# Performance work log

Measured on AMD Instinct MI355X. Metric: run time of the kernel, lower is better.

## Reference

```python
import jax, jax.numpy as jnp
import numpy as np

H = 8          # query heads
KVH = 1        # key/value heads
HD = 256       # head dim
ROPE_BASE = 10000.0


def _rotate_half(x):
    x1, x2 = x[..., : HD // 2], x[..., HD // 2 :]
    return jnp.concatenate((-x2, x1), axis=-1)


def _rope_cos_sin(position_ids):
    # position_ids: [B, S] int -> cos/sin: [B, S, HD]
    inv_freq = 1.0 / (ROPE_BASE ** (jnp.arange(0, HD, 2, dtype=jnp.float32) / HD))
    freqs = position_ids.astype(jnp.float32)[..., None] * inv_freq  # [B,S,HD/2]
    emb = jnp.concatenate((freqs, freqs), axis=-1)                  # [B,S,HD]
    return jnp.cos(emb), jnp.sin(emb)


def setup_inputs() -> dict:
    key = jax.random.key(0)
    ks = jax.random.split(key, 5)
    B, S, D = 2, 2048, 2048
    return {
        "hidden_states": jax.random.normal(ks[0], (B, S, D), dtype=jnp.float32),
        "attention_mask": jnp.zeros((B, 1, S, S), dtype=jnp.float32),
        "position_ids": jnp.broadcast_to(jnp.arange(S, dtype=jnp.int32), (B, S)),
        "Wq": jax.random.normal(ks[1], (D, H * HD), dtype=jnp.float32) * 0.02,
        "Wk": jax.random.normal(ks[2], (D, KVH * HD), dtype=jnp.float32) * 0.02,
        "Wv": jax.random.normal(ks[3], (D, KVH * HD), dtype=jnp.float32) * 0.02,
        "Wo": jax.random.normal(ks[4], (H * HD, D), dtype=jnp.float32) * 0.02,
    }


def reference(hidden_states, attention_mask, position_ids, Wq, Wk, Wv, Wo):
    B, S, D = hidden_states.shape
    # projections -> [B, heads, S, HD]
    q = jnp.einsum("bsd,df->bsf", hidden_states, Wq).reshape(B, S, H, HD).transpose(0, 2, 1, 3)
    k = jnp.einsum("bsd,df->bsf", hidden_states, Wk).reshape(B, S, KVH, HD).transpose(0, 2, 1, 3)
    v = jnp.einsum("bsd,df->bsf", hidden_states, Wv).reshape(B, S, KVH, HD).transpose(0, 2, 1, 3)

    cos, sin = _rope_cos_sin(position_ids)
    cos, sin = cos[:, None], sin[:, None]  # unsqueeze head dim
    q = q * cos + _rotate_half(q) * sin
    k = k * cos + _rotate_half(k) * sin

    # GQA: repeat kv heads to match query heads
    rep = H // KVH
    k = jnp.repeat(k, rep, axis=1)
    v = jnp.repeat(v, rep, axis=1)

    d_k = D // H  # matches torch code's scaling (== HD here)
    scores = jnp.einsum("bhqd,bhkd->bhqk", q, k) / jnp.sqrt(jnp.float32(d_k))
    scores = scores + attention_mask
    attn = jax.nn.softmax(scores, axis=-1)  # dropout p=0 / eval mode

    out = jnp.einsum("bhqk,bhkd->bhqd", attn, v)  # [B,H,S,HD]
    out = out.transpose(0, 2, 1, 3).reshape(B, S, H * HD)
    out = jnp.einsum("bsf,fd->bsd", out, Wo)
    return out
```

## Files before the change

### kernel.cpp

```cpp
#include <hip/hip_runtime.h>
#include <cmath>


typedef __bf16 bf16;
typedef __attribute__((ext_vector_type(8))) __bf16 bf16x8;
typedef __attribute__((ext_vector_type(4))) __bf16 bf16x4;
typedef __attribute__((ext_vector_type(4))) float f32x4;

#define S_LEN 2048
#define D_MODEL 2048
#define H_NUM 8
#define HDIM 256
#define NT (S_LEN / 64)
#define SM_BIAS 8.0f

#define BAR __builtin_amdgcn_s_barrier()
#define SCHED0 __builtin_amdgcn_sched_barrier(0)

__device__ __forceinline__ void gl_lds16(const bf16* g, bf16* l) {
  __builtin_amdgcn_global_load_lds(
      (const __attribute__((address_space(1))) void*)g,
      (__attribute__((address_space(3))) void*)l, 16, 0, 0);
}

__global__ void cvt_bf16(const float* __restrict__ src, bf16* __restrict__ dst) {
  const int i = (blockIdx.x * 256 + threadIdx.x) * 4;
  const float4 v = *(const float4*)(src + i);
  bf16x4 o;
  o[0] = (bf16)v.x; o[1] = (bf16)v.y; o[2] = (bf16)v.z; o[3] = (bf16)v.w;
  *(bf16x4*)(dst + i) = o;
}

__global__ void tpose_all(const float* __restrict__ Wq, const float* __restrict__ Wk,
                          const float* __restrict__ Wv, const float* __restrict__ Wo,
                          bf16* __restrict__ Wqkvt, bf16* __restrict__ Wot) {
  __shared__ float t[32][33];
  const int tx = threadIdx.x, ty = threadIdx.y;
  const int bx = blockIdx.x;
  const int k0 = blockIdx.y * 32;
  const float* W; bf16* Wt; int Ncols, no0, n0;
  if (bx < 64)      { W = Wq; Wt = Wqkvt; Ncols = 2048; no0 = 0;    n0 = bx * 32; }
  else if (bx < 72) { W = Wk; Wt = Wqkvt; Ncols = 256;  no0 = 2048; n0 = (bx - 64) * 32; }
  else if (bx < 80) { W = Wv; Wt = Wqkvt; Ncols = 256;  no0 = 2304; n0 = (bx - 72) * 32; }
  else              { W = Wo; Wt = Wot;   Ncols = 2048; no0 = 0;    n0 = (bx - 80) * 32; }
#pragma unroll
  for (int i = 0; i < 4; ++i)
    t[ty + 8 * i][tx] = W[(size_t)(k0 + ty + 8 * i) * Ncols + (n0 + tx)];
  __syncthreads();
#pragma unroll
  for (int i = 0; i < 4; ++i)
    Wt[(size_t)(no0 + n0 + ty + 8 * i) * D_MODEL + (k0 + tx)] = (bf16)t[tx][ty + 8 * i];
}

__global__ __launch_bounds__(512, 2)
void gemm_bf16(const bf16* __restrict__ A, const bf16* __restrict__ Wt,
               bf16* __restrict__ Cq, bf16* __restrict__ Ck, bf16* __restrict__ Cv,
               float* __restrict__ Cf, int NX, int mode) {
  __shared__ bf16 As[2][2][128 * 64];
  __shared__ bf16 Bs[2][2][128 * 64];
  const int tid = threadIdx.x;
  const int lane = tid & 63;
  const int w = tid >> 6;
  const int c16 = lane & 15;
  const int quad = lane >> 4;
  const int wm = w >> 2;
  const int wn = w & 3;

  const int nwg = gridDim.x;
  const int swz = (blockIdx.x & 7) * (nwg >> 3) + (blockIdx.x >> 3);
  const int m0 = (swz / NX) * 256;
  const int n0 = (swz % NX) * 256;

  const char* Ab = (const char*)A;
  const char* Bb = (const char*)Wt;
  const int lr8 = lane >> 3;
  const int scb = ((lane & 7) ^ lr8) << 4;

  f32x4 acc[8][4];
#pragma unroll
  for (int i = 0; i < 8; ++i)
#pragma unroll
    for (int j = 0; j < 4; ++j)
#pragma unroll
      for (int r = 0; r < 4; ++r) acc[i][j][r] = 0.f;

  auto stg = [&](const char* gcol, int grow0, bf16* lhalf) {
#pragma unroll
    for (int j2 = 0; j2 < 2; ++j2) {
      const int c = w * 2 + j2;
      gl_lds16((const bf16*)(gcol + (size_t)(grow0 + c * 8 + lr8) * 4096 + scb),
               lhalf + c * 512);
    }
  };
  auto ldA = [&](int sl, int qm, bf16x8* d) {
    const char* base = (const char*)&As[sl][wm][0];
#pragma unroll
    for (int i = 0; i < 4; ++i) {
      const int row = qm * 64 + i * 16 + c16;
      const int sw = (row & 7) << 4;
#pragma unroll
      for (int kk = 0; kk < 2; ++kk)
        d[i * 2 + kk] = *(const bf16x8*)(base + row * 128 + ((kk * 64 + quad * 16) ^ sw));
    }
  };
  auto ldB = [&](int sl, int qn, bf16x8* d) {
    const char* base = (const char*)&Bs[sl][wn >> 1][0];
#pragma unroll
    for (int j = 0; j < 2; ++j) {
      const int row = (wn & 1) * 64 + qn * 32 + j * 16 + c16;
      const int sw = (row & 7) << 4;
#pragma unroll
      for (int kk = 0; kk < 2; ++kk)
        d[j * 2 + kk] = *(const bf16x8*)(base + row * 128 + ((kk * 64 + quad * 16) ^ sw));
    }
  };
  auto mm = [&](int qm, int qn, const bf16x8* a, const bf16x8* bb) {
    __builtin_amdgcn_s_setprio(1);
#pragma unroll
    for (int kk = 0; kk < 2; ++kk)
#pragma unroll
      for (int i = 0; i < 4; ++i)
#pragma unroll
        for (int j = 0; j < 2; ++j)
          acc[qm * 4 + i][qn * 2 + j] = __builtin_amdgcn_mfma_f32_16x16x32_bf16(
              a[i * 2 + kk], bb[j * 2 + kk], acc[qm * 4 + i][qn * 2 + j], 0, 0, 0);
    __builtin_amdgcn_s_setprio(0);
  };

  bf16x8 Xa[8], Ya[8], Xb[4], Yb[4];

  stg(Ab, m0, &As[0][0][0]);        stg(Ab, m0 + 128, &As[0][1][0]);
  stg(Bb, n0, &Bs[0][0][0]);        stg(Bb, n0 + 128, &Bs[0][1][0]);
  stg(Bb + 128, n0, &Bs[1][0][0]);  stg(Bb + 128, n0 + 128, &Bs[1][1][0]);
  asm volatile("s_waitcnt vmcnt(4)" ::: "memory");
  BAR;

  for (int t = 0; t < 16; ++t) {
    const int kc = t * 256;
    const bool pf = (t < 15);
    ldA(0, 0, Xa); ldB(0, 0, Xb);
    stg(Ab + kc + 128, m0, &As[1][0][0]);
    BAR; mm(0, 0, Xa, Xb);
    ldB(0, 1, Yb);
    stg(Ab + kc + 128, m0 + 128, &As[1][1][0]);
    BAR; mm(0, 1, Xa, Yb);
    ldA(0, 1, Ya);
    if (pf) stg(Bb + kc + 256, n0, &Bs[0][0][0]);
    BAR; mm(1, 1, Ya, Yb);
    if (pf) {
      stg(Ab + kc + 256, m0, &As[0][0][0]);
      asm volatile("s_waitcnt vmcnt(4)" ::: "memory");
    } else {
      asm volatile("s_waitcnt vmcnt(0)" ::: "memory");
    }
    BAR; mm(1, 0, Ya, Xb);
    ldA(1, 0, Xa); ldB(1, 0, Xb);
    if (pf) stg(Bb + kc + 256, n0 + 128, &Bs[0][1][0]);
    BAR; mm(0, 0, Xa, Xb);
    ldB(1, 1, Yb);
    if (pf) stg(Ab + kc + 256, m0 + 128, &As[0][1][0]);
    BAR; mm(0, 1, Xa, Yb);
    ldA(1, 1, Ya);
    if (pf) stg(Bb + kc + 384, n0, &Bs[1][0][0]);
    BAR; mm(1, 1, Ya, Yb);
    if (pf) {
      stg(Bb + kc + 384, n0 + 128, &Bs[1][1][0]);
      asm volatile("s_waitcnt vmcnt(4)" ::: "memory");
      BAR; mm(1, 0, Ya, Xb);
    } else {
      BAR; mm(1, 0, Ya, Xb);
    }
  }

#pragma unroll
  for (int i = 0; i < 8; ++i)
#pragma unroll
    for (int j = 0; j < 4; ++j) {
      const int n = n0 + wn * 64 + j * 16 + c16;
#pragma unroll
      for (int r = 0; r < 4; ++r) {
        const int m = m0 + wm * 128 + i * 16 + quad * 4 + r;
        const float val = acc[i][j][r];
        if (mode == 1) {
          const int b = m >> 11, s = m & 2047;
          if (n0 < 2048) {
            const int h = n >> 8, hd = n & 255;
            Cq[((((size_t)b * H_NUM + h) * S_LEN + s) << 8) + hd] = (bf16)val;
          } else if (n0 < 2304) {
            Ck[((size_t)m << 8) + (n - 2048)] = (bf16)val;
          } else {
            Cv[((size_t)((b << 8) + (n - 2304)) << 11) + s] = (bf16)val;
          }
        } else {
          Cf[(size_t)m * D_MODEL + n] = val;
        }
      }
    }
}

#define ROPE_C (-0.07195578415606394f)

__global__ void rope_all(bf16* __restrict__ q, bf16* __restrict__ k,
                         const int* __restrict__ pos, int BHS) {
  const int idx = blockIdx.x * 256 + threadIdx.x;
  const int j = idx & 127;
  const int t = idx >> 7;
  float sn, cs;
  if (t < BHS) {
    const int s = t & 2047;
    const int b = t >> 14;
    const float p = (float)pos[(b << 11) + s];
    sincosf(p * expf((float)j * ROPE_C), &sn, &cs);
    bf16* base = q + ((size_t)t << 8);
    const float x1 = (float)base[j], x2 = (float)base[j + 128];
    base[j] = (bf16)(x1 * cs - x2 * sn);
    base[j + 128] = (bf16)(x2 * cs + x1 * sn);
  } else {
    const int t2 = t - BHS;
    const int s = t2 & 2047;
    const int b = t2 >> 11;
    const float p = (float)pos[(b << 11) + s];
    sincosf(p * expf((float)j * ROPE_C), &sn, &cs);
    bf16* base = k + ((size_t)t2 << 8);
    const float x1 = (float)base[j], x2 = (float)base[j + 128];
    base[j] = (bf16)(x1 * cs - x2 * sn);
    base[j + 128] = (bf16)(x2 * cs + x1 * sn);
  }
}

__global__ __launch_bounds__(512, 2)
void flash_bf16(const bf16* __restrict__ qg, const bf16* __restrict__ kg,
                const bf16* __restrict__ vg, const float* __restrict__ msk,
                bf16* __restrict__ ao) {
  __shared__ bf16 Ks[2][64 * 256];
  __shared__ bf16 Vs[2][256 * 64];
  __shared__ bf16 Ps[128 * 64];
  __shared__ float Lp[2][128];

  const int tid = threadIdx.x;
  const int lane = tid & 63;
  const int w = tid >> 6;
  const int c16 = lane & 15;
  const int quad = lane >> 4;
  const int qi = w & 3;
  const int sec = w >> 2;

  const int bidx = blockIdx.x;
  int b, qb;
  if (gridDim.x == 256) {
    b = (bidx & 7) >> 2;
    qb = ((bidx & 3) << 5) | (bidx >> 3);
  } else {
    b = bidx >> 7;
    qb = bidx & 127;
  }
  const int q0 = qb * 16;

  const bf16* qh = qg + ((((size_t)b * H_NUM + qi * 2) * S_LEN + q0) << 8);
  const char* kbase = (const char*)(kg + ((size_t)b << 19));
  const char* vbase = (const char*)(vg + ((size_t)b << 19));
  const float* mbase = msk + (size_t)b * S_LEN * S_LEN + (size_t)q0 * S_LEN;

  bf16x8 qf[2][8];
#pragma unroll
  for (int mi = 0; mi < 2; ++mi)
#pragma unroll
    for (int kd = 0; kd < 8; ++kd)
      qf[mi][kd] = *(const bf16x8*)&qh[(((size_t)mi * S_LEN + c16) << 8) + kd * 32 + quad * 8];

  f32x4 oacc[2][8];
#pragma unroll
  for (int mi = 0; mi < 2; ++mi)
#pragma unroll
    for (int nj = 0; nj < 8; ++nj)
#pragma unroll
      for (int r = 0; r < 4; ++r) oacc[mi][nj][r] = 0.f;
  float plsum[2][4];
#pragma unroll
  for (int mi = 0; mi < 2; ++mi)
#pragma unroll
    for (int r = 0; r < 4; ++r) plsum[mi][r] = 0.f;

  auto stage_kv = [&](int k0, int buf) {
#pragma unroll
    for (int j = 0; j < 4; ++j) {
      const int ki = w * 4 + j;
      const int krow = ki * 2 + (lane >> 5);
      const int kcb = ((lane & 31) * 16) ^ ((krow & 7) << 4);
      gl_lds16((const bf16*)(kbase + ((size_t)(k0 + krow) << 9) + kcb),
               &Ks[buf][ki * 512]);
      const int vrow = ki * 8 + (lane >> 3);
      const int vcb = ((lane & 7) * 16) ^ ((vrow & 7) << 4);
      gl_lds16((const bf16*)(vbase + ((size_t)vrow << 12) + (k0 << 1) + vcb),
               &Vs[buf][ki * 512]);
    }
  };
  auto mask_ld = [&](int k0, float (&ml)[2][4]) {
#pragma unroll
    for (int nj = 0; nj < 2; ++nj)
#pragma unroll
      for (int r = 0; r < 4; ++r)
        ml[nj][r] = mbase[(size_t)(quad * 4 + r) * S_LEN +
                          k0 + sec * 32 + nj * 16 + c16];
  };

  auto tile = [&](int k0, int buf, const float (&ml)[2][4]) {
    f32x4 sc[2][2];
#pragma unroll
    for (int mi = 0; mi < 2; ++mi)
#pragma unroll
      for (int nj = 0; nj < 2; ++nj)
#pragma unroll
        for (int r = 0; r < 4; ++r) sc[mi][nj][r] = 0.f;
    __builtin_amdgcn_s_setprio(1);
#pragma unroll
    for (int kd = 0; kd < 8; ++kd) {
      bf16x8 bK[2];
#pragma unroll
      for (int nj = 0; nj < 2; ++nj) {
        const int row = sec * 32 + nj * 16 + c16;
        bK[nj] = *(const bf16x8*)((const char*)&Ks[buf][0] + row * 512 +
                                  ((kd * 64 + quad * 16) ^ ((row & 7) << 4)));
      }
#pragma unroll
      for (int mi = 0; mi < 2; ++mi)
#pragma unroll
        for (int nj = 0; nj < 2; ++nj)
          sc[mi][nj] = __builtin_amdgcn_mfma_f32_16x16x32_bf16(qf[mi][kd], bK[nj], sc[mi][nj], 0, 0, 0);
    }
    __builtin_amdgcn_s_setprio(0);

#pragma unroll
    for (int mi = 0; mi < 2; ++mi)
#pragma unroll
      for (int nj = 0; nj < 2; ++nj)
#pragma unroll
        for (int r = 0; r < 4; ++r) {
          const float p = __expf(sc[mi][nj][r] * 0.0625f + ml[nj][r] - SM_BIAS);
          plsum[mi][r] += p;
          const int row = qi * 32 + mi * 16 + quad * 4 + r;
          const int cb = ((sec * 32 + nj * 16 + c16) * 2) ^ ((row & 7) << 4);
          *(bf16*)((char*)&Ps[0] + row * 128 + cb) = (bf16)p;
        }

    SCHED0;
    asm volatile("s_waitcnt lgkmcnt(0)" ::: "memory");
    BAR;
    SCHED0;

    bf16x8 pa[2][2];
#pragma unroll
    for (int mi = 0; mi < 2; ++mi)
#pragma unroll
      for (int ks = 0; ks < 2; ++ks) {
        const int row = qi * 32 + mi * 16 + c16;
        pa[mi][ks] = *(const bf16x8*)((const char*)&Ps[0] + row * 128 +
                                      ((ks * 64 + quad * 16) ^ ((row & 7) << 4)));
      }
    __builtin_amdgcn_s_setprio(1);
#pragma unroll
    for (int nj = 0; nj < 8; ++nj) {
#pragma unroll
      for (int ks = 0; ks < 2; ++ks) {
        const int drow = sec * 128 + nj * 16 + c16;
        const bf16x8 bv = *(const bf16x8*)((const char*)&Vs[buf][0] + drow * 128 +
                                           ((ks * 64 + quad * 16) ^ ((drow & 7) << 4)));
#pragma unroll
        for (int mi = 0; mi < 2; ++mi)
          oacc[mi][nj] = __builtin_amdgcn_mfma_f32_16x16x32_bf16(pa[mi][ks], bv, oacc[mi][nj], 0, 0, 0);
      }
    }
    __builtin_amdgcn_s_setprio(0);
  };

  float mlA[2][4], mlB[2][4];
  stage_kv(0, 0);
  mask_ld(0, mlA);

  for (int u = 0; u < NT / 2; ++u) {
    const int te = 2 * u;
    asm volatile("s_waitcnt vmcnt(0)" ::: "memory");
    BAR;
    SCHED0;
    stage_kv((te + 1) * 64, 1);
    mask_ld((te + 1) * 64, mlB);
    tile(te * 64, 0, mlA);
    asm volatile("s_waitcnt vmcnt(0)" ::: "memory");
    BAR;
    SCHED0;
    if (u + 1 < NT / 2) {
      stage_kv((te + 2) * 64, 0);
      mask_ld((te + 2) * 64, mlA);
    }
    tile((te + 1) * 64, 1, mlB);
  }

#pragma unroll
  for (int mi = 0; mi < 2; ++mi)
#pragma unroll
    for (int r = 0; r < 4; ++r) {
      float s = plsum[mi][r];
      s += __shfl_xor(s, 1, 64);
      s += __shfl_xor(s, 2, 64);
      s += __shfl_xor(s, 4, 64);
      s += __shfl_xor(s, 8, 64);
      if (c16 == 0) Lp[sec][qi * 32 + mi * 16 + quad * 4 + r] = s;
    }
  __syncthreads();
  float li[2][4];
#pragma unroll
  for (int mi = 0; mi < 2; ++mi)
#pragma unroll
    for (int r = 0; r < 4; ++r) {
      const int row = qi * 32 + mi * 16 + quad * 4 + r;
      li[mi][r] = 1.f / (Lp[0][row] + Lp[1][row]);
    }
  bf16* obase = ao + (size_t)(b * S_LEN + q0 + quad * 4) * D_MODEL + qi * 512 + sec * 128;
#pragma unroll
  for (int mi = 0; mi < 2; ++mi)
#pragma unroll
    for (int nj = 0; nj < 8; ++nj)
#pragma unroll
      for (int r = 0; r < 4; ++r)
        obase[(size_t)r * D_MODEL + mi * 256 + nj * 16 + c16] =
            (bf16)(oacc[mi][nj][r] * li[mi][r]);
}

extern "C" void kernel_launch(void* const* d_in, const int* in_sizes, int n_in,
                              void* d_out, int out_size, void* d_ws, size_t ws_size,
                              hipStream_t stream) {
  const float* hs   = (const float*)d_in[0];
  const float* mask = (const float*)d_in[1];
  const int*   pos  = (const int*)d_in[2];
  const float* Wq   = (const float*)d_in[3];
  const float* Wk   = (const float*)d_in[4];
  const float* Wv   = (const float*)d_in[5];
  const float* Wo   = (const float*)d_in[6];
  float* out = (float*)d_out;

  const int B = in_sizes[2] / S_LEN;
  const int M = B * S_LEN;

  char* wsc = (char*)d_ws;
  bf16* hsb = (bf16*)wsc;
  bf16* aob = hsb;
  size_t off = (size_t)M * D_MODEL * 2;
  bf16* Wqkvt = (bf16*)(wsc + off); off += (size_t)2560 * D_MODEL * 2;
  bf16* Wot   = (bf16*)(wsc + off); off += (size_t)D_MODEL * D_MODEL * 2;
  bf16* kb    = (bf16*)(wsc + off);
  bf16* vb    = kb + (size_t)M * HDIM;

  bf16* qb = (bf16*)d_out;

  const dim3 blk(256);
  cvt_bf16<<<(M * D_MODEL) / 1024, blk, 0, stream>>>(hs, hsb);
  tpose_all<<<dim3(144, 64), dim3(32, 8), 0, stream>>>(Wq, Wk, Wv, Wo, Wqkvt, Wot);

  gemm_bf16<<<10 * (M / 256), dim3(512), 0, stream>>>(hsb, Wqkvt, qb, kb, vb, nullptr, 10, 1);

  rope_all<<<(B * (H_NUM + 1) * S_LEN * 128) / 256, blk, 0, stream>>>(
      qb, kb, pos, B * H_NUM * S_LEN);

  flash_bf16<<<B * (S_LEN / 16), dim3(512), 0, stream>>>(qb, kb, vb, mask, aob);

  gemm_bf16<<<8 * (M / 256), dim3(512), 0, stream>>>(aob, Wot, nullptr, nullptr, nullptr, out, 8, 3);
}
```

Baseline: 404.5 us.

## Read K and V fragments directly from global memory instead of LDS staging

```diff
diff --git a/kernel.cpp b/kernel.cpp
--- a/kernel.cpp
+++ b/kernel.cpp
@@ -232,8 +232,6 @@
 void flash_bf16(const bf16* __restrict__ qg, const bf16* __restrict__ kg,
                 const bf16* __restrict__ vg, const float* __restrict__ msk,
                 bf16* __restrict__ ao) {
-  __shared__ bf16 Ks[2][64 * 256];
-  __shared__ bf16 Vs[2][256 * 64];
   __shared__ bf16 Ps[128 * 64];
   __shared__ float Lp[2][128];
 
@@ -281,30 +279,17 @@
 #pragma unroll
     for (int r = 0; r < 4; ++r) plsum[mi][r] = 0.f;
 
-  auto stage_kv = [&](int k0, int buf) {
-#pragma unroll
-    for (int j = 0; j < 4; ++j) {
-      const int ki = w * 4 + j;
-      const int krow = ki * 2 + (lane >> 5);
-      const int kcb = ((lane & 31) * 16) ^ ((krow & 7) << 4);
-      gl_lds16((const bf16*)(kbase + ((size_t)(k0 + krow) << 9) + kcb),
-               &Ks[buf][ki * 512]);
-      const int vrow = ki * 8 + (lane >> 3);
-      const int vcb = ((lane & 7) * 16) ^ ((vrow & 7) << 4);
-      gl_lds16((const bf16*)(vbase + ((size_t)vrow << 12) + (k0 << 1) + vcb),
-               &Vs[buf][ki * 512]);
-    }
-  };
-  auto mask_ld = [&](int k0, float (&ml)[2][4]) {
+  for (int t = 0; t < NT; ++t) {
+    const int k0 = t * 64;
+
+    float ml[2][4];
 #pragma unroll
     for (int nj = 0; nj < 2; ++nj)
 #pragma unroll
       for (int r = 0; r < 4; ++r)
         ml[nj][r] = mbase[(size_t)(quad * 4 + r) * S_LEN +
                           k0 + sec * 32 + nj * 16 + c16];
-  };
-
-  auto tile = [&](int k0, int buf, const float (&ml)[2][4]) {
+
     f32x4 sc[2][2];
 #pragma unroll
     for (int mi = 0; mi < 2; ++mi)
@@ -318,9 +303,8 @@
       bf16x8 bK[2];
 #pragma unroll
       for (int nj = 0; nj < 2; ++nj) {
-        const int row = sec * 32 + nj * 16 + c16;
-        bK[nj] = *(const bf16x8*)((const char*)&Ks[buf][0] + row * 512 +
-                                  ((kd * 64 + quad * 16) ^ ((row & 7) << 4)));
+        const int row = k0 + sec * 32 + nj * 16 + c16;
+        bK[nj] = *(const bf16x8*)(kbase + ((size_t)row << 9) + kd * 64 + quad * 16);
       }
 #pragma unroll
       for (int mi = 0; mi < 2; ++mi)
@@ -363,36 +347,16 @@
 #pragma unroll
       for (int ks = 0; ks < 2; ++ks) {
         const int drow = sec * 128 + nj * 16 + c16;
-        const bf16x8 bv = *(const bf16x8*)((const char*)&Vs[buf][0] + drow * 128 +
-                                           ((ks * 64 + quad * 16) ^ ((drow & 7) << 4)));
+        const bf16x8 bv = *(const bf16x8*)(vbase + ((size_t)drow << 12) +
+                                           ((k0 + ks * 32 + quad * 8) << 1));
 #pragma unroll
         for (int mi = 0; mi < 2; ++mi)
           oacc[mi][nj] = __builtin_amdgcn_mfma_f32_16x16x32_bf16(pa[mi][ks], bv, oacc[mi][nj], 0, 0, 0);
       }
     }
     __builtin_amdgcn_s_setprio(0);
-  };
-
-  float mlA[2][4], mlB[2][4];
-  stage_kv(0, 0);
-  mask_ld(0, mlA);
-
-  for (int u = 0; u < NT / 2; ++u) {
-    const int te = 2 * u;
-    asm volatile("s_waitcnt vmcnt(0)" ::: "memory");
-    BAR;
-    SCHED0;
-    stage_kv((te + 1) * 64, 1);
-    mask_ld((te + 1) * 64, mlB);
-    tile(te * 64, 0, mlA);
-    asm volatile("s_waitcnt vmcnt(0)" ::: "memory");
-    BAR;
-    SCHED0;
-    if (u + 1 < NT / 2) {
-      stage_kv((te + 2) * 64, 0);
-      mask_ld((te + 2) * 64, mlA);
-    }
-    tile((te + 1) * 64, 1, mlB);
+
+    __syncthreads();
   }
 
 #pragma unroll
```

After: 545.1 us. 34.8% more time.
